# Optimization experiments

Measured on AMD Instinct MI355X. Metric: run time of the kernel, lower is better.

## Reference

```python
import jax, jax.numpy as jnp
import numpy as np
from jax import lax

G = 32          # growthrate / num_features
KS = 3          # filter_size
PAD = (KS - 1) // 2
NUM_LAYERS = 4


def _conv2d(x, w, b):
    # x: [B, Cin, H, W], w: [Cout, Cin, k, k]
    y = lax.conv_general_dilated(
        x, w, window_strides=(1, 1), padding=[(PAD, PAD), (PAD, PAD)],
        dimension_numbers=("NCHW", "OIHW", "NCHW"))
    return y + b[None, :, None, None]


def _scan_cell(xs, w, b):
    # xs: [T, B, Cin, H, W]; ConvLSTM-like cell: A = tanh(conv(cat(x, c)))
    # split A -> (ai[G], af[G], ao[1]); h = ai; c_next = sigmoid(ao) * af
    T, B, _, H, W = xs.shape
    c0 = jnp.zeros((B, G, H, W), xs.dtype)

    def step(c, x):
        A = jnp.tanh(_conv2d(jnp.concatenate([x, c], axis=1), w, b))
        h = A[:, :G]
        cand = A[:, G:2 * G]
        gate = jax.nn.sigmoid(A[:, 2 * G:])
        c_next = gate * cand
        return c_next, (h, c_next, gate)

    _, (hs, cs, gs) = lax.scan(step, c0, xs)
    return hs, cs, gs  # each [T, B, G or 1, H, W]


def setup_inputs() -> dict:
    key = jax.random.key(0)
    ks = jax.random.split(key, 1 + 4 * NUM_LAYERS)
    T, B, C, H, W = 8, 4, 32, 64, 64
    inp = {"x": jax.random.normal(ks[0], (T, B, C, H, W), jnp.float32)}
    cin = [C] + [2 * l * G for l in range(1, NUM_LAYERS)]  # [32, 64, 128, 192]
    cout = 2 * G + 1
    for l in range(NUM_LAYERS):
        ci = cin[l] + G
        inp[f"wf{l}"] = jax.random.normal(ks[1 + 4 * l], (cout, ci, KS, KS), jnp.float32) * 0.02
        inp[f"bf{l}"] = jax.random.normal(ks[2 + 4 * l], (cout,), jnp.float32) * 0.02
        inp[f"wb{l}"] = jax.random.normal(ks[3 + 4 * l], (cout, ci, KS, KS), jnp.float32) * 0.02
        inp[f"bb{l}"] = jax.random.normal(ks[4 + 4 * l], (cout,), jnp.float32) * 0.02
    return inp


def reference(x, wf0, bf0, wb0, bb0, wf1, bf1, wb1, bb1,
              wf2, bf2, wb2, bb2, wf3, bf3, wb3, bb3):
    fwd = [(wf0, bf0), (wf1, bf1), (wf2, bf2), (wf3, bf3)]
    bwd = [(wb0, bb0), (wb1, bb1), (wb2, bb2), (wb3, bb3)]
    output = x  # [T, B, C, H, W]
    lr_h, lr_c, lr_g = [], [], []
    for l in range(NUM_LAYERS):
        hf, cf, gf = _scan_cell(output, *fwd[l])
        hb, _, _ = _scan_cell(output[::-1], *bwd[l])
        hb = hb[::-1]  # align backward pass to original time order
        cur = jnp.concatenate([hf, hb], axis=2)  # [T, B, 2G, H, W]
        output = cur if l == 0 else jnp.concatenate([output, cur], axis=2)
        lr_h.append(hf[-1]); lr_c.append(cf[-1]); lr_g.append(gf[-1])
    return (output, jnp.stack(lr_h), jnp.stack(lr_c), jnp.stack(lr_g))
```

## Files before the change

### kernel.cpp

```cpp
#include <hip/hip_runtime.h>
#include <math.h>

#define T_STEPS 8
#define HW 4096
#define XSTR 192
#define FR_ROW 4352

typedef unsigned short u16;
typedef __attribute__((ext_vector_type(8))) short short8;
typedef __attribute__((ext_vector_type(4))) short short4v;
typedef __attribute__((ext_vector_type(4))) float f32x4;

__device__ __forceinline__ u16 f2bf(float f) {
    unsigned u = __builtin_bit_cast(unsigned, f);
    u += 0x7fffu + ((u >> 16) & 1u);
    return (u16)(u >> 16);
}
__device__ __forceinline__ float bf2f(u16 h) {
    unsigned u = ((unsigned)h) << 16;
    return __builtin_bit_cast(float, u);
}
__device__ __forceinline__ float ftanh(float x) {
    float e = __expf(2.f * x);
    return 1.f - 2.f * __builtin_amdgcn_rcpf(e + 1.f);
}
__device__ __forceinline__ float fsigm(float x) {
    return __builtin_amdgcn_rcpf(1.f + __expf(-x));
}

__global__ __launch_bounds__(256) void transpose_halo(
    const float* __restrict__ src, u16* __restrict__ XT, int src_ctot)
{
    __shared__ float tile[32][257];
    const int img = blockIdx.z;
    const int px0 = blockIdx.x * 256;
    const float* s = src + (size_t)img * src_ctot * HW + px0;
    #pragma unroll
    for (int c = 0; c < 32; ++c)
        tile[c][threadIdx.x] = s[(size_t)c * HW + threadIdx.x];
    __syncthreads();
    const int c = threadIdx.x & 31, pb = threadIdx.x >> 5;
    const int r0 = px0 >> 6;
    for (int p = pb; p < 256; p += 8) {
        int row = r0 + (p >> 6), col = p & 63;
        XT[((size_t)img * 4356 + (row + 1) * 66 + col + 1) * XSTR + c] = f2bf(tile[c][p]);
    }
}

struct WP { const float* p[8]; };

__global__ __launch_bounds__(256) void prep_w_all(WP wp, u16* __restrict__ Wr)
{
    int idx = blockIdx.x * 256 + threadIdx.x;
    if (idx >= 783360) return;
    const int offs[5] = {0, 92160, 230400, 460800, 783360};
    const int cit[4]  = {64, 96, 160, 224};
    int lay = 0;
    while (idx >= offs[lay + 1]) ++lay;
    int li = idx - offs[lay];
    int ci_total = cit[lay];
    int ci = li % ci_total;
    int rest = li / ci_total;
    int co = rest % 80; rest /= 80;
    int tap = rest % 9;
    int dir = rest / 9;
    const float* w = wp.p[lay * 2 + dir];
    float v = (co < 65) ? w[((size_t)co * ci_total + ci) * 9 + tap] : 0.f;
    Wr[idx] = f2bf(v);
}

__global__ __launch_bounds__(512, 2) void convx_mfma(
    const u16* __restrict__ XT, const u16* __restrict__ Wr,
    const float* __restrict__ b_f, const float* __restrict__ b_b,
    u16* __restrict__ convx, int cin, int ci_total)
{
    __shared__ u16 xs[2][6 * 66 * 32];
    const int tid = threadIdx.x;
    const int l = tid & 63, wv = tid >> 6;
    const int g = l >> 4, ln16 = l & 15;
    const int img = blockIdx.z;
    const int dir = wv & 1;
    const int wrow = wv >> 1;
    const int r0  = blockIdx.x * 4;
    const int orow = r0 + wrow;

    const float* bias = dir ? b_b : b_f;
    f32x4 acc[5][4];
    #pragma unroll
    for (int mt = 0; mt < 5; ++mt)
        #pragma unroll
        for (int r = 0; r < 4; ++r) {
            int co = mt * 16 + g * 4 + r;
            float bv = (co < 65) ? bias[co] : 0.f;
            #pragma unroll
            for (int nt = 0; nt < 4; ++nt) acc[mt][nt][r] = bv;
        }

    const u16* wdir = Wr + (size_t)dir * 9 * 80 * ci_total + g * 8;
    const u16* xim  = XT + (size_t)img * 4356 * XSTR;
    const int nstage = (cin >= 64) ? 3168 : 1584;

    for (int ch0 = 0; ch0 < cin; ch0 += 64) {
        __syncthreads();
        #pragma unroll
        for (int k = 0; k < 7; ++k) {
            int idx = k * 512 + tid;
            if (idx < nstage) {
                int bufi = (idx >= 1584) ? 1 : 0;
                int ii = idx - bufi * 1584;
                int seg = ii & 3, pr = ii >> 2;
                short8 v = *(const short8*)(xim + (size_t)(r0 * 66 + pr) * XSTR
                                            + ch0 + bufi * 32 + seg * 8);
                *(short8*)(xs[bufi] + (size_t)ii * 8) = v;
            }
        }
        __syncthreads();

        #pragma unroll
        for (int cc = 0; cc < 2; ++cc) {
            const int ch = ch0 + cc * 32;
            if (ch >= cin) break;
            #pragma unroll
            for (int ky = 0; ky < 3; ++ky) {
                #pragma unroll
                for (int kx = 0; kx < 3; ++kx) {
                    const int tap = ky * 3 + kx;
                    const u16* xb = xs[cc] + ((size_t)((wrow + ky) * 66 + ln16 + kx)) * 32 + g * 8;
                    short8 bv0 = *(const short8*)(xb);
                    short8 bv1 = *(const short8*)(xb + 16 * 32);
                    short8 bv2 = *(const short8*)(xb + 32 * 32);
                    short8 bv3 = *(const short8*)(xb + 48 * 32);
                    const u16* wb_ = wdir + ((size_t)tap * 80 + ln16) * ci_total + ch;
                    #pragma unroll
                    for (int mt = 0; mt < 5; ++mt) {
                        short8 af = *(const short8*)(wb_ + (size_t)mt * 16 * ci_total);
                        acc[mt][0] = __builtin_amdgcn_mfma_f32_16x16x32_bf16(af, bv0, acc[mt][0], 0, 0, 0);
                        acc[mt][1] = __builtin_amdgcn_mfma_f32_16x16x32_bf16(af, bv1, acc[mt][1], 0, 0, 0);
                        acc[mt][2] = __builtin_amdgcn_mfma_f32_16x16x32_bf16(af, bv2, acc[mt][2], 0, 0, 0);
                        acc[mt][3] = __builtin_amdgcn_mfma_f32_16x16x32_bf16(af, bv3, acc[mt][3], 0, 0, 0);
                    }
                }
            }
        }
    }

    const int zimg = dir * 32 + img;
    u16* cb = convx + ((size_t)zimg * 64 + orow) * FR_ROW;
    #pragma unroll
    for (int mt = 0; mt < 4; ++mt)
        #pragma unroll
        for (int nt = 0; nt < 4; ++nt) {
            short4v pk;
            #pragma unroll
            for (int r = 0; r < 4; ++r) pk[r] = (short)f2bf(acc[mt][nt][r]);
            *(short4v*)(cb + (size_t)(nt * 4 + mt) * 256 + l * 4) = pk;
        }
    if (g == 0) {
        #pragma unroll
        for (int nt = 0; nt < 4; ++nt) {
            short4v pk;
            #pragma unroll
            for (int r = 0; r < 4; ++r) pk[r] = (short)f2bf(acc[4][nt][r]);
            *(short4v*)(cb + 4096 + nt * 64 + ln16 * 4) = pk;
        }
    }
}

__global__ __launch_bounds__(512) void rec_mfma(
    const u16* __restrict__ cT_in, u16* __restrict__ cT_out,
    const u16* __restrict__ Wr, const u16* __restrict__ convx,
    float* __restrict__ out_t,
    float* __restrict__ lrh, float* __restrict__ lrc, float* __restrict__ lrg,
    u16* __restrict__ XT,
    int cin, int ci_total, int layer, int step)
{
    const int tid = threadIdx.x;
    const int l = tid & 63, w = tid >> 6;
    const int g = l >> 4, ln16 = l & 15;
    const int role = w & 1, ws = w >> 1;
    const int z = blockIdx.z;
    const int dir = z >> 2, b = z & 3;
    const int t = dir ? (7 - step) : step;
    const int row  = blockIdx.x * 2 + (ws >> 1);
    const int nb   = (ws & 1) * 2;
    const int col0 = nb * 16;
    const int zimg = dir * 32 + t * 4 + b;
    const int m0 = role * 2;

    const u16* cxb = convx + ((size_t)zimg * 64 + row) * FR_ROW;
    f32x4 acc[3][2];
    #pragma unroll
    for (int j = 0; j < 2; ++j)
        #pragma unroll
        for (int nt = 0; nt < 2; ++nt) {
            short4v pk = *(const short4v*)(cxb + (size_t)((nb + nt) * 4 + (m0 + j)) * 256 + l * 4);
            #pragma unroll
            for (int r = 0; r < 4; ++r) acc[j][nt][r] = bf2f((u16)pk[r]);
        }
    #pragma unroll
    for (int nt = 0; nt < 2; ++nt) {
        if (g == 0) {
            short4v pk = *(const short4v*)(cxb + 4096 + (nb + nt) * 64 + ln16 * 4);
            #pragma unroll
            for (int r = 0; r < 4; ++r) acc[2][nt][r] = bf2f((u16)pk[r]);
        } else {
            #pragma unroll
            for (int r = 0; r < 4; ++r) acc[2][nt][r] = 0.f;
        }
    }

    if (step > 0) {
        const u16* wdir = Wr + (size_t)dir * 9 * 80 * ci_total + cin + g * 8;
        const u16* cim  = cT_in + (size_t)z * 4356 * 32 + g * 8;
        __builtin_amdgcn_s_setprio(1);
        #pragma unroll
        for (int ky = 0; ky < 3; ++ky) {
            #pragma unroll
            for (int kx = 0; kx < 3; ++kx) {
                const int tap = ky * 3 + kx;
                const u16* xb_ = cim + (size_t)((row + ky) * 66 + col0 + ln16 + kx) * 32;
                short8 bv0 = *(const short8*)(xb_);
                short8 bv1 = *(const short8*)(xb_ + 16 * 32);
                const u16* wb_ = wdir + ((size_t)tap * 80 + ln16) * ci_total;
                short8 af0 = *(const short8*)(wb_ + (size_t)(m0    ) * 16 * ci_total);
                short8 af1 = *(const short8*)(wb_ + (size_t)(m0 + 1) * 16 * ci_total);
                short8 af4 = *(const short8*)(wb_ + (size_t)4 * 16 * ci_total);
                acc[0][0] = __builtin_amdgcn_mfma_f32_16x16x32_bf16(af0, bv0, acc[0][0], 0, 0, 0);
                acc[0][1] = __builtin_amdgcn_mfma_f32_16x16x32_bf16(af0, bv1, acc[0][1], 0, 0, 0);
                acc[1][0] = __builtin_amdgcn_mfma_f32_16x16x32_bf16(af1, bv0, acc[1][0], 0, 0, 0);
                acc[1][1] = __builtin_amdgcn_mfma_f32_16x16x32_bf16(af1, bv1, acc[1][1], 0, 0, 0);
                acc[2][0] = __builtin_amdgcn_mfma_f32_16x16x32_bf16(af4, bv0, acc[2][0], 0, 0, 0);
                acc[2][1] = __builtin_amdgcn_mfma_f32_16x16x32_bf16(af4, bv1, acc[2][1], 0, 0, 0);
            }
        }
        __builtin_amdgcn_s_setprio(0);
    }

    const bool last_f = (dir == 0) && (step == 7);
    float val[2], gv[2];
    #pragma unroll
    for (int nt = 0; nt < 2; ++nt) {
        val[nt] = fsigm(ftanh(acc[2][nt][0]));
        gv[nt]  = __shfl(val[nt], ln16);
    }

    if (role == 0) {
        const size_t obase = (size_t)(t * 4 + b) * 256 + 64 * layer + dir * 32;
        const int chb = 64 * layer + dir * 32;
        #pragma unroll
        for (int j = 0; j < 2; ++j)
            #pragma unroll
            for (int nt = 0; nt < 2; ++nt) {
                int px = row * 64 + col0 + nt * 16 + ln16;
                short4v pkh;
                #pragma unroll
                for (int r = 0; r < 4; ++r) {
                    int co = j * 16 + g * 4 + r;
                    float v = ftanh(acc[j][nt][r]);
                    out_t[(obase + co) * HW + px] = v;
                    pkh[r] = (short)f2bf(v);
                    if (last_f) lrh[((size_t)(layer * 4 + b) * 32 + co) * HW + px] = v;
                }
                if (layer < 3)
                    *(short4v*)(XT + ((size_t)(t * 4 + b) * 4356 + (row + 1) * 66 +
                                      (col0 + nt * 16 + ln16 + 1)) * XSTR + chb + j * 16 + g * 4) = pkh;
            }
        if (last_f && g == 0) {
            #pragma unroll
            for (int nt = 0; nt < 2; ++nt)
                lrg[(size_t)(layer * 4 + b) * HW + row * 64 + col0 + nt * 16 + ln16] = val[nt];
        }
    } else {
        #pragma unroll
        for (int j = 0; j < 2; ++j)
            #pragma unroll
            for (int nt = 0; nt < 2; ++nt) {
                short4v pk;
                #pragma unroll
                for (int r = 0; r < 4; ++r) {
                    int k = j * 16 + g * 4 + r;
                    float c = gv[nt] * ftanh(acc[j][nt][r]);
                    pk[r] = (short)f2bf(c);
                    if (last_f)
                        lrc[((size_t)(layer * 4 + b) * 32 + k) * HW + row * 64 + col0 + nt * 16 + ln16] = c;
                }
                int colh = col0 + nt * 16 + ln16 + 1;
                *(short4v*)(cT_out + ((size_t)z * 4356 + (row + 1) * 66 + colh) * 32 + j * 16 + g * 4) = pk;
            }
    }
}

extern "C" void kernel_launch(void* const* d_in, const int* in_sizes, int n_in,
                              void* d_out, int out_size, void* d_ws, size_t ws_size,
                              hipStream_t stream)
{
    const float* x = (const float*)d_in[0];
    float* out = (float*)d_out;
    float* lrh = out + (size_t)33554432;
    float* lrc = lrh + (size_t)2097152;
    float* lrg = lrc + (size_t)2097152;

    char* ws = (char*)d_ws;
    u16* convx = (u16*)ws;
    size_t off = 35651584 + 4096;
    u16* cT_a = (u16*)(ws + off); off += 2230272;
    u16* cT_b = (u16*)(ws + off); off += 2230272;
    u16* XT = (u16*)(ws + off); off += 53526528;
    u16* Wr = (u16*)(ws + off);

    static const int offs[4] = {0, 92160, 230400, 460800};

    hipMemsetAsync(XT, 0, 53526528, stream);
    hipMemsetAsync(cT_a, 0, 2230272, stream);
    hipMemsetAsync(cT_b, 0, 2230272, stream);
    transpose_halo<<<dim3(16, 1, 32), 256, 0, stream>>>(x, XT, 32);

    WP wp;
    for (int l = 0; l < 4; ++l) {
        wp.p[l * 2]     = (const float*)d_in[1 + 4 * l];
        wp.p[l * 2 + 1] = (const float*)d_in[3 + 4 * l];
    }
    prep_w_all<<<dim3((783360 + 255) / 256), 256, 0, stream>>>(wp, Wr);

    for (int l = 0; l < 4; ++l) {
        const float* bf = (const float*)d_in[2 + 4 * l];
        const float* bb = (const float*)d_in[4 + 4 * l];
        int cin = (l == 0) ? 32 : 64 * l;
        int ci_total = cin + 32;
        const u16* Wrl = Wr + offs[l];

        convx_mfma<<<dim3(16, 1, 32), 512, 0, stream>>>(XT, Wrl, bf, bb, convx, cin, ci_total);

        for (int s = 0; s < 8; ++s) {
            const u16* cin_p = (s & 1) ? cT_b : cT_a;
            u16* cout_p      = (s & 1) ? cT_a : cT_b;
            rec_mfma<<<dim3(32, 1, 8), 512, 0, stream>>>(
                cin_p, cout_p, Wrl, convx, out, lrh, lrc, lrg, XT,
                cin, ci_total, l, s);
        }
    }
}
```

Baseline: 668.1 us.

## Shrink convx LDS staging to one 32-channel buffer and defer bias-add in step kernel

The input-projection conv kernel now stages one 32-channel slab of the input halo in LDS per iteration instead of two, which halves shared memory per block and may raise occupancy, but doubles the number of sync/load phases. The recurrent step kernel keeps the precomputed conv contribution as packed bf16 and adds it after the MFMA loop, so accumulators start at zero and the conversion moves off the critical path. It also skips writing the next cell state on the final step, where it is never read.

```diff
diff --git a/kernel.cpp b/kernel.cpp
--- a/kernel.cpp
+++ b/kernel.cpp
@@ -74,7 +74,7 @@
     const float* __restrict__ b_f, const float* __restrict__ b_b,
     u16* __restrict__ convx, int cin, int ci_total)
 {
-    __shared__ u16 xs[2][6 * 66 * 32];
+    __shared__ u16 xs[6 * 66 * 32];
     const int tid = threadIdx.x;
     const int l = tid & 63, wv = tid >> 6;
     const int g = l >> 4, ln16 = l & 15;
@@ -98,47 +98,39 @@
 
     const u16* wdir = Wr + (size_t)dir * 9 * 80 * ci_total + g * 8;
     const u16* xim  = XT + (size_t)img * 4356 * XSTR;
-    const int nstage = (cin >= 64) ? 3168 : 1584;
-
-    for (int ch0 = 0; ch0 < cin; ch0 += 64) {
+
+    for (int ch = 0; ch < cin; ch += 32) {
         __syncthreads();
         #pragma unroll
-        for (int k = 0; k < 7; ++k) {
+        for (int k = 0; k < 4; ++k) {
             int idx = k * 512 + tid;
-            if (idx < nstage) {
-                int bufi = (idx >= 1584) ? 1 : 0;
-                int ii = idx - bufi * 1584;
-                int seg = ii & 3, pr = ii >> 2;
-                short8 v = *(const short8*)(xim + (size_t)(r0 * 66 + pr) * XSTR
-                                            + ch0 + bufi * 32 + seg * 8);
-                *(short8*)(xs[bufi] + (size_t)ii * 8) = v;
+            if (idx < 1584) {
+                int seg = idx & 3;
+                int pr  = idx >> 2;
+                short8 v = *(const short8*)(xim + (size_t)(r0 * 66 + pr) * XSTR + ch + seg * 8);
+                *(short8*)(xs + (size_t)idx * 8) = v;
             }
         }
         __syncthreads();
 
         #pragma unroll
-        for (int cc = 0; cc < 2; ++cc) {
-            const int ch = ch0 + cc * 32;
-            if (ch >= cin) break;
-            #pragma unroll
-            for (int ky = 0; ky < 3; ++ky) {
+        for (int ky = 0; ky < 3; ++ky) {
+            #pragma unroll
+            for (int kx = 0; kx < 3; ++kx) {
+                const int tap = ky * 3 + kx;
+                const u16* xb = xs + ((size_t)((wrow + ky) * 66 + ln16 + kx)) * 32 + g * 8;
+                short8 bv0 = *(const short8*)(xb);
+                short8 bv1 = *(const short8*)(xb + 16 * 32);
+                short8 bv2 = *(const short8*)(xb + 32 * 32);
+                short8 bv3 = *(const short8*)(xb + 48 * 32);
+                const u16* wb_ = wdir + ((size_t)tap * 80 + ln16) * ci_total + ch;
                 #pragma unroll
-                for (int kx = 0; kx < 3; ++kx) {
-                    const int tap = ky * 3 + kx;
-                    const u16* xb = xs[cc] + ((size_t)((wrow + ky) * 66 + ln16 + kx)) * 32 + g * 8;
-                    short8 bv0 = *(const short8*)(xb);
-                    short8 bv1 = *(const short8*)(xb + 16 * 32);
-                    short8 bv2 = *(const short8*)(xb + 32 * 32);
-                    short8 bv3 = *(const short8*)(xb + 48 * 32);
-                    const u16* wb_ = wdir + ((size_t)tap * 80 + ln16) * ci_total + ch;
-                    #pragma unroll
-                    for (int mt = 0; mt < 5; ++mt) {
-                        short8 af = *(const short8*)(wb_ + (size_t)mt * 16 * ci_total);
-                        acc[mt][0] = __builtin_amdgcn_mfma_f32_16x16x32_bf16(af, bv0, acc[mt][0], 0, 0, 0);
-                        acc[mt][1] = __builtin_amdgcn_mfma_f32_16x16x32_bf16(af, bv1, acc[mt][1], 0, 0, 0);
-                        acc[mt][2] = __builtin_amdgcn_mfma_f32_16x16x32_bf16(af, bv2, acc[mt][2], 0, 0, 0);
-                        acc[mt][3] = __builtin_amdgcn_mfma_f32_16x16x32_bf16(af, bv3, acc[mt][3], 0, 0, 0);
-                    }
+                for (int mt = 0; mt < 5; ++mt) {
+                    short8 af = *(const short8*)(wb_ + (size_t)mt * 16 * ci_total);
+                    acc[mt][0] = __builtin_amdgcn_mfma_f32_16x16x32_bf16(af, bv0, acc[mt][0], 0, 0, 0);
+                    acc[mt][1] = __builtin_amdgcn_mfma_f32_16x16x32_bf16(af, bv1, acc[mt][1], 0, 0, 0);
+                    acc[mt][2] = __builtin_amdgcn_mfma_f32_16x16x32_bf16(af, bv2, acc[mt][2], 0, 0, 0);
+                    acc[mt][3] = __builtin_amdgcn_mfma_f32_16x16x32_bf16(af, bv3, acc[mt][3], 0, 0, 0);
                 }
             }
         }
@@ -188,27 +180,19 @@
     const int m0 = role * 2;
 
     const u16* cxb = convx + ((size_t)zimg * 64 + row) * FR_ROW;
-    f32x4 acc[3][2];
+    short4v cx[3][2];
     #pragma unroll
     for (int j = 0; j < 2; ++j)
         #pragma unroll
-        for (int nt = 0; nt < 2; ++nt) {
-            short4v pk = *(const short4v*)(cxb + (size_t)((nb + nt) * 4 + (m0 + j)) * 256 + l * 4);
-            #pragma unroll
-            for (int r = 0; r < 4; ++r) acc[j][nt][r] = bf2f((u16)pk[r]);
-        }
-    #pragma unroll
-    for (int nt = 0; nt < 2; ++nt) {
-        if (g == 0) {
-            short4v pk = *(const short4v*)(cxb + 4096 + (nb + nt) * 64 + ln16 * 4);
-            #pragma unroll
-            for (int r = 0; r < 4; ++r) acc[2][nt][r] = bf2f((u16)pk[r]);
-        } else {
-            #pragma unroll
-            for (int r = 0; r < 4; ++r) acc[2][nt][r] = 0.f;
-        }
-    }
-
+        for (int nt = 0; nt < 2; ++nt)
+            cx[j][nt] = *(const short4v*)(cxb + (size_t)((nb + nt) * 4 + (m0 + j)) * 256 + l * 4);
+    #pragma unroll
+    for (int nt = 0; nt < 2; ++nt)
+        cx[2][nt] = (g == 0)
+            ? *(const short4v*)(cxb + 4096 + (nb + nt) * 64 + ln16 * 4)
+            : (short4v){0, 0, 0, 0};
+
+    f32x4 acc[3][2] = {};
     if (step > 0) {
         const u16* wdir = Wr + (size_t)dir * 9 * 80 * ci_total + cin + g * 8;
         const u16* cim  = cT_in + (size_t)z * 4356 * 32 + g * 8;
@@ -240,7 +224,7 @@
     float val[2], gv[2];
     #pragma unroll
     for (int nt = 0; nt < 2; ++nt) {
-        val[nt] = fsigm(ftanh(acc[2][nt][0]));
+        val[nt] = fsigm(ftanh(acc[2][nt][0] + bf2f((u16)cx[2][nt][0])));
         gv[nt]  = __shfl(val[nt], ln16);
     }
 
@@ -256,7 +240,7 @@
                 #pragma unroll
                 for (int r = 0; r < 4; ++r) {
                     int co = j * 16 + g * 4 + r;
-                    float v = ftanh(acc[j][nt][r]);
+                    float v = ftanh(acc[j][nt][r] + bf2f((u16)cx[j][nt][r]));
                     out_t[(obase + co) * HW + px] = v;
                     pkh[r] = (short)f2bf(v);
                     if (last_f) lrh[((size_t)(layer * 4 + b) * 32 + co) * HW + px] = v;
@@ -279,13 +263,15 @@
                 #pragma unroll
                 for (int r = 0; r < 4; ++r) {
                     int k = j * 16 + g * 4 + r;
-                    float c = gv[nt] * ftanh(acc[j][nt][r]);
+                    float c = gv[nt] * ftanh(acc[j][nt][r] + bf2f((u16)cx[j][nt][r]));
                     pk[r] = (short)f2bf(c);
                     if (last_f)
                         lrc[((size_t)(layer * 4 + b) * 32 + k) * HW + row * 64 + col0 + nt * 16 + ln16] = c;
                 }
-                int colh = col0 + nt * 16 + ln16 + 1;
-                *(short4v*)(cT_out + ((size_t)z * 4356 + (row + 1) * 66 + colh) * 32 + j * 16 + g * 4) = pk;
+                if (step < 7) {
+                    int colh = col0 + nt * 16 + ln16 + 1;
+                    *(short4v*)(cT_out + ((size_t)z * 4356 + (row + 1) * 66 + colh) * 32 + j * 16 + g * 4) = pk;
+                }
             }
     }
 }
```

After: 576.6 us. 1.16x faster.
